# Optimization experiments

Hardware: AMD Instinct MI355X
Metric: run time of the kernel (lower is better)

The kernel has to match this reference:

```python
import jax, jax.numpy as jnp
import numpy as np

MUL = 128                      # shared multiplicity (MACE channels)
IN_DIMS = (1, 3, 5)            # 0e, 1o, 2e -> d_in_single = 9
OUT_DIMS = (1, 3)              # 0e, 1o -> d_out_single = 4
OUT_SLICES = ((0, 1), (1, 4))
ENTRIES = ((1, 0), (1, 1), (2, 0), (2, 1), (3, 0), (3, 1))  # (nu, out_idx)
N_BASIS = (1, 1, 2, 2, 3, 3)
N_NODES = 2048
N_ELEM = 10


def _to_per_mul(x):
    # (n, sum mul*dim) -> (n, mul, d_in_single)
    n = x.shape[0]
    pieces, off = [], 0
    for d in IN_DIMS:
        pieces.append(x[:, off:off + MUL * d].reshape(n, MUL, d))
        off += MUL * d
    return jnp.concatenate(pieces, axis=-1)


def _from_per_mul(x):
    # (n, mul, d_out_single) -> (n, sum mul*dim)
    n = x.shape[0]
    pieces = []
    for (lo, hi), d in zip(OUT_SLICES, OUT_DIMS):
        pieces.append(x[:, :, lo:hi].reshape(n, MUL * d))
    return jnp.concatenate(pieces, axis=-1)


def _symmetric_contraction(feats, species, bases, weights):
    n = feats.shape[0]
    out = jnp.zeros((n, MUL, sum(OUT_DIMS)), dtype=feats.dtype)
    for (nu, out_idx), basis, w in zip(ENTRIES, bases, weights):
        basis = jax.lax.stop_gradient(basis).astype(feats.dtype)
        # chain of nu symmetric contractions of basis against feats
        tmp = jnp.einsum('a...,ima->im...', basis, feats)  # (n, mul, 9^{nu-1}, nb, d)
        for _ in range(nu - 1):
            tmp = jnp.einsum('ima...,ima->im...', tmp, feats)
        w_per_node = w[species]                           # (n, nb, mul)
        contracted = jnp.einsum('nsm,nmsp->nmp', w_per_node, tmp)
        lo, hi = OUT_SLICES[out_idx]
        out = out.at[:, :, lo:hi].add(contracted)
    return out


def setup_inputs() -> dict:
    key = jax.random.key(0)
    ks = jax.random.split(key, 16)
    d_in = sum(IN_DIMS)
    inp = {
        'node_feats': jax.random.normal(ks[0], (N_NODES, MUL * d_in), jnp.float32),
        'species': jax.random.randint(ks[1], (N_NODES,), 0, N_ELEM),
    }
    names_b = ('b10', 'b11', 'b20', 'b21', 'b30', 'b31')
    names_w = ('w10', 'w11', 'w20', 'w21', 'w30', 'w31')
    for i, ((nu, oi), nb) in enumerate(zip(ENTRIES, N_BASIS)):
        bshape = (d_in,) * nu + (nb, OUT_DIMS[oi])
        inp[names_b[i]] = jax.random.normal(ks[2 + i], bshape, jnp.float32)
        scale = 1.0 / np.sqrt(nb)
        inp[names_w[i]] = jax.random.normal(ks[8 + i], (N_ELEM, nb, MUL), jnp.float32) * scale
    return inp


def reference(node_feats, species, b10, b11, b20, b21, b30, b31,
              w10, w11, w20, w21, w30, w31):
    feats = _to_per_mul(node_feats)
    out = _symmetric_contraction(
        feats, species,
        [b10, b11, b20, b21, b30, b31],
        [w10, w11, w20, w21, w30, w31])
    return _from_per_mul(out)
```

## Files before the change

### kernel.cpp

```cpp
#include <hip/hip_runtime.h>

#define NTH 256
#define N_NODES 2048

#define G3_OFF 0
#define G2_OFF 1980
#define G1_OFF 2340
#define TAB_FLOATS 2376

__global__ void mace_prep(
    const float* __restrict__ b10, const float* __restrict__ b11,
    const float* __restrict__ b20, const float* __restrict__ b21,
    const float* __restrict__ b30, const float* __restrict__ b31,
    float* __restrict__ tab)
{
    const int tid = threadIdx.x;
    if (tid < 165) {
        int i = 0, j = 0, k = 0;
        {
            int c = 0;
            for (int ii = 0; ii < 9; ii++)
                for (int jj = ii; jj < 9; jj++)
                    for (int kk = jj; kk < 9; kk++) {
                        if (c == tid) { i = ii; j = jj; k = kk; }
                        c++;
                    }
        }
        float s[12];
        #pragma unroll
        for (int q = 0; q < 12; q++) s[q] = 0.f;
        auto add3 = [&](int a, int b, int c2) {
            int o30 = ((a * 9 + b) * 9 + c2) * 3;
            int o31 = o30 * 3;
            #pragma unroll
            for (int q = 0; q < 3; q++) s[q] += b30[o30 + q];
            #pragma unroll
            for (int q = 0; q < 9; q++) s[3 + q] += b31[o31 + q];
        };
        if (i == j && j == k) { add3(i, j, k); }
        else if (i == j)      { add3(i, i, k); add3(i, k, i); add3(k, i, i); }
        else if (j == k)      { add3(i, j, j); add3(j, i, j); add3(j, j, i); }
        else { add3(i,j,k); add3(i,k,j); add3(j,i,k); add3(j,k,i); add3(k,i,j); add3(k,j,i); }
        #pragma unroll
        for (int q = 0; q < 12; q++) tab[G3_OFF + tid * 12 + q] = s[q];
    } else if (tid < 210) {
        int t = tid - 165;
        int i = 0, j = 0;
        {
            int c = 0;
            for (int ii = 0; ii < 9; ii++)
                for (int jj = ii; jj < 9; jj++) {
                    if (c == t) { i = ii; j = jj; }
                    c++;
                }
        }
        float s[8];
        #pragma unroll
        for (int q = 0; q < 8; q++) s[q] = 0.f;
        auto add2 = [&](int a, int b) {
            int o20 = (a * 9 + b) * 2;
            int o21 = o20 * 3;
            #pragma unroll
            for (int q = 0; q < 2; q++) s[q] += b20[o20 + q];
            #pragma unroll
            for (int q = 0; q < 6; q++) s[2 + q] += b21[o21 + q];
        };
        if (i == j) add2(i, i); else { add2(i, j); add2(j, i); }
        #pragma unroll
        for (int q = 0; q < 8; q++) tab[G2_OFF + t * 8 + q] = s[q];
    } else if (tid < 219) {
        int a = tid - 210;
        tab[G1_OFF + a * 4 + 0] = b10[a];
        #pragma unroll
        for (int p = 0; p < 3; p++) tab[G1_OFF + a * 4 + 1 + p] = b11[a * 3 + p];
    }
}

__global__ __launch_bounds__(NTH, 2) void mace_sc_kernel(
    const float* __restrict__ nf, const int* __restrict__ spec,
    const float* __restrict__ w10, const float* __restrict__ w11,
    const float* __restrict__ w20, const float* __restrict__ w21,
    const float* __restrict__ w30, const float* __restrict__ w31,
    const float* __restrict__ tab, float* __restrict__ out)
{
    const int g    = blockIdx.x * NTH + threadIdx.x;
    const int node = g >> 7;
    const int m    = g & 127;

    const float* nfp = nf + node * 1152;
    float f[9];
    f[0] = nfp[m];
    #pragma unroll
    for (int j = 0; j < 3; j++) f[1 + j] = nfp[128 + m * 3 + j];
    #pragma unroll
    for (int j = 0; j < 5; j++) f[4 + j] = nfp[512 + m * 5 + j];

    const int z = spec[node];

    float acc[4];
    #pragma unroll
    for (int p = 0; p < 4; p++) acc[p] = 0.f;

    {
        float t3[12];
        #pragma unroll
        for (int q = 0; q < 12; q++) t3[q] = 0.f;

        int t = 0;
        #pragma unroll
        for (int i = 0; i < 9; i++) {
            #pragma unroll
            for (int j = i; j < 9; j++) {
                const float fij = f[i] * f[j];
                #pragma unroll
                for (int k = j; k < 9; k++) {
                    const float* c = &tab[G3_OFF + t * 12];
                    const float m3 = fij * f[k];
                    #pragma unroll
                    for (int q = 0; q < 12; q++) t3[q] = fmaf(c[q], m3, t3[q]);
                    t++;
                }
            }
        }
        const float* w30z = w30 + z * 3 * 128;
        const float* w31z = w31 + z * 3 * 128;
        #pragma unroll
        for (int s = 0; s < 3; s++) {
            const float wv = w30z[s * 128 + m];
            acc[0] = fmaf(wv, t3[s], acc[0]);
            const float wu = w31z[s * 128 + m];
            acc[1] = fmaf(wu, t3[3 + s * 3 + 0], acc[1]);
            acc[2] = fmaf(wu, t3[3 + s * 3 + 1], acc[2]);
            acc[3] = fmaf(wu, t3[3 + s * 3 + 2], acc[3]);
        }
    }

    {
        float t2[8];
        #pragma unroll
        for (int q = 0; q < 8; q++) t2[q] = 0.f;

        int t = 0;
        #pragma unroll
        for (int i = 0; i < 9; i++) {
            #pragma unroll
            for (int j = i; j < 9; j++) {
                const float* c = &tab[G2_OFF + t * 8];
                const float m2 = f[i] * f[j];
                #pragma unroll
                for (int q = 0; q < 8; q++) t2[q] = fmaf(c[q], m2, t2[q]);
                t++;
            }
        }
        const float* w20z = w20 + z * 2 * 128;
        const float* w21z = w21 + z * 2 * 128;
        #pragma unroll
        for (int s = 0; s < 2; s++) {
            const float wv = w20z[s * 128 + m];
            acc[0] = fmaf(wv, t2[s], acc[0]);
            const float wu = w21z[s * 128 + m];
            acc[1] = fmaf(wu, t2[2 + s * 3 + 0], acc[1]);
            acc[2] = fmaf(wu, t2[2 + s * 3 + 1], acc[2]);
            acc[3] = fmaf(wu, t2[2 + s * 3 + 2], acc[3]);
        }
    }

    {
        float t1[4];
        #pragma unroll
        for (int q = 0; q < 4; q++) t1[q] = 0.f;

        #pragma unroll
        for (int a = 0; a < 9; a++) {
            const float* c = &tab[G1_OFF + a * 4];
            #pragma unroll
            for (int q = 0; q < 4; q++) t1[q] = fmaf(c[q], f[a], t1[q]);
        }
        const float wv = w10[z * 128 + m];
        acc[0] = fmaf(wv, t1[0], acc[0]);
        const float wu = w11[z * 128 + m];
        acc[1] = fmaf(wu, t1[1], acc[1]);
        acc[2] = fmaf(wu, t1[2], acc[2]);
        acc[3] = fmaf(wu, t1[3], acc[3]);
    }

    float* op = out + node * 512;
    op[m] = acc[0];
    #pragma unroll
    for (int p = 0; p < 3; p++) op[128 + m * 3 + p] = acc[1 + p];
}

extern "C" void kernel_launch(void* const* d_in, const int* in_sizes, int n_in,
                              void* d_out, int out_size, void* d_ws, size_t ws_size,
                              hipStream_t stream) {
    const float* nf  = (const float*)d_in[0];
    const int* spec  = (const int*)d_in[1];
    const float* b10 = (const float*)d_in[2];
    const float* w10 = (const float*)d_in[3];
    const float* b11 = (const float*)d_in[4];
    const float* w11 = (const float*)d_in[5];
    const float* b20 = (const float*)d_in[6];
    const float* w20 = (const float*)d_in[7];
    const float* b21 = (const float*)d_in[8];
    const float* w21 = (const float*)d_in[9];
    const float* b30 = (const float*)d_in[10];
    const float* w30 = (const float*)d_in[11];
    const float* b31 = (const float*)d_in[12];
    const float* w31 = (const float*)d_in[13];
    float* out = (float*)d_out;
    float* tab = (float*)d_ws;

    mace_prep<<<1, 256, 0, stream>>>(b10, b11, b20, b21, b30, b31, tab);

    const int n_threads = N_NODES * 128;
    const int grid = n_threads / NTH;
    mace_sc_kernel<<<grid, NTH, 0, stream>>>(
        nf, spec, w10, w11, w20, w21, w30, w31, tab, out);
}
```

Before: 116.7 us.

## Split output channels across two thread halves per node with shared-memory reduction

Each node now gets a 256-thread block, and two threads share each channel. Each thread computes half of the combined coefficient table columns (6 of 12 for nu=3, 4 of 8 for nu=2, 2 of 4 for nu=1), and the prep kernel writes the tables in split A/B halves to match. Partial accumulators from the second half are reduced through shared memory before the first half writes the output. This doubles the thread count, cuts per-thread FMA work and register pressure, and adds occupancy, at the cost of recomputing the monomials twice, loading the features twice, and one block barrier.

```diff
diff --git a/kernel.cpp b/kernel.cpp
--- a/kernel.cpp
+++ b/kernel.cpp
@@ -3,9 +3,12 @@
 #define NTH 256
 #define N_NODES 2048
 
-#define G3_OFF 0
-#define G2_OFF 1980
-#define G1_OFF 2340
+#define G3A_OFF 0
+#define G3B_OFF 990
+#define G2A_OFF 1980
+#define G2B_OFF 2160
+#define G1A_OFF 2340
+#define G1B_OFF 2358
 #define TAB_FLOATS 2376
 
 __global__ void mace_prep(
@@ -42,7 +45,10 @@
         else if (j == k)      { add3(i, j, j); add3(j, i, j); add3(j, j, i); }
         else { add3(i,j,k); add3(i,k,j); add3(j,i,k); add3(j,k,i); add3(k,i,j); add3(k,j,i); }
         #pragma unroll
-        for (int q = 0; q < 12; q++) tab[G3_OFF + tid * 12 + q] = s[q];
+        for (int q = 0; q < 6; q++) {
+            tab[G3A_OFF + tid * 6 + q] = s[q];
+            tab[G3B_OFF + tid * 6 + q] = s[6 + q];
+        }
     } else if (tid < 210) {
         int t = tid - 165;
         int i = 0, j = 0;
@@ -67,12 +73,16 @@
         };
         if (i == j) add2(i, i); else { add2(i, j); add2(j, i); }
         #pragma unroll
-        for (int q = 0; q < 8; q++) tab[G2_OFF + t * 8 + q] = s[q];
+        for (int q = 0; q < 4; q++) {
+            tab[G2A_OFF + t * 4 + q] = s[q];
+            tab[G2B_OFF + t * 4 + q] = s[4 + q];
+        }
     } else if (tid < 219) {
         int a = tid - 210;
-        tab[G1_OFF + a * 4 + 0] = b10[a];
-        #pragma unroll
-        for (int p = 0; p < 3; p++) tab[G1_OFF + a * 4 + 1 + p] = b11[a * 3 + p];
+        tab[G1A_OFF + a * 2 + 0] = b10[a];
+        tab[G1A_OFF + a * 2 + 1] = b11[a * 3 + 0];
+        tab[G1B_OFF + a * 2 + 0] = b11[a * 3 + 1];
+        tab[G1B_OFF + a * 2 + 1] = b11[a * 3 + 2];
     }
 }
 
@@ -83,9 +93,13 @@
     const float* __restrict__ w30, const float* __restrict__ w31,
     const float* __restrict__ tab, float* __restrict__ out)
 {
-    const int g    = blockIdx.x * NTH + threadIdx.x;
-    const int node = g >> 7;
-    const int m    = g & 127;
+    __shared__ float part[4][128];
+
+    const int node = blockIdx.x;
+    const int tid  = threadIdx.x;
+    const int w    = tid >> 6;
+    const int h    = w >> 1;
+    const int m    = ((w & 1) << 6) | (tid & 63);
 
     const float* nfp = nf + node * 1152;
     float f[9];
@@ -102,9 +116,10 @@
     for (int p = 0; p < 4; p++) acc[p] = 0.f;
 
     {
-        float t3[12];
-        #pragma unroll
-        for (int q = 0; q < 12; q++) t3[q] = 0.f;
+        const float* g3 = tab + (h ? G3B_OFF : G3A_OFF);
+        float t3[6];
+        #pragma unroll
+        for (int q = 0; q < 6; q++) t3[q] = 0.f;
 
         int t = 0;
         #pragma unroll
@@ -114,80 +129,107 @@
                 const float fij = f[i] * f[j];
                 #pragma unroll
                 for (int k = j; k < 9; k++) {
-                    const float* c = &tab[G3_OFF + t * 12];
+                    const float* c = &g3[t * 6];
                     const float m3 = fij * f[k];
                     #pragma unroll
-                    for (int q = 0; q < 12; q++) t3[q] = fmaf(c[q], m3, t3[q]);
+                    for (int q = 0; q < 6; q++) t3[q] = fmaf(c[q], m3, t3[q]);
                     t++;
                 }
             }
         }
-        const float* w30z = w30 + z * 3 * 128;
-        const float* w31z = w31 + z * 3 * 128;
-        #pragma unroll
-        for (int s = 0; s < 3; s++) {
-            const float wv = w30z[s * 128 + m];
-            acc[0] = fmaf(wv, t3[s], acc[0]);
-            const float wu = w31z[s * 128 + m];
-            acc[1] = fmaf(wu, t3[3 + s * 3 + 0], acc[1]);
-            acc[2] = fmaf(wu, t3[3 + s * 3 + 1], acc[2]);
-            acc[3] = fmaf(wu, t3[3 + s * 3 + 2], acc[3]);
+        if (h == 0) {
+            const float* w30z = w30 + z * 384;
+            const float* w31z = w31 + z * 384;
+            #pragma unroll
+            for (int s = 0; s < 3; s++)
+                acc[0] = fmaf(w30z[s * 128 + m], t3[s], acc[0]);
+            const float wu = w31z[m];
+            acc[1] = fmaf(wu, t3[3], acc[1]);
+            acc[2] = fmaf(wu, t3[4], acc[2]);
+            acc[3] = fmaf(wu, t3[5], acc[3]);
+        } else {
+            const float* w31z = w31 + z * 384;
+            const float wu1 = w31z[128 + m];
+            const float wu2 = w31z[256 + m];
+            acc[1] = fmaf(wu1, t3[0], acc[1]);
+            acc[2] = fmaf(wu1, t3[1], acc[2]);
+            acc[3] = fmaf(wu1, t3[2], acc[3]);
+            acc[1] = fmaf(wu2, t3[3], acc[1]);
+            acc[2] = fmaf(wu2, t3[4], acc[2]);
+            acc[3] = fmaf(wu2, t3[5], acc[3]);
         }
     }
 
     {
-        float t2[8];
-        #pragma unroll
-        for (int q = 0; q < 8; q++) t2[q] = 0.f;
+        const float* g2 = tab + (h ? G2B_OFF : G2A_OFF);
+        float t2[4];
+        #pragma unroll
+        for (int q = 0; q < 4; q++) t2[q] = 0.f;
 
         int t = 0;
         #pragma unroll
         for (int i = 0; i < 9; i++) {
             #pragma unroll
             for (int j = i; j < 9; j++) {
-                const float* c = &tab[G2_OFF + t * 8];
+                const float* c = &g2[t * 4];
                 const float m2 = f[i] * f[j];
                 #pragma unroll
-                for (int q = 0; q < 8; q++) t2[q] = fmaf(c[q], m2, t2[q]);
+                for (int q = 0; q < 4; q++) t2[q] = fmaf(c[q], m2, t2[q]);
                 t++;
             }
         }
-        const float* w20z = w20 + z * 2 * 128;
-        const float* w21z = w21 + z * 2 * 128;
-        #pragma unroll
-        for (int s = 0; s < 2; s++) {
-            const float wv = w20z[s * 128 + m];
-            acc[0] = fmaf(wv, t2[s], acc[0]);
-            const float wu = w21z[s * 128 + m];
-            acc[1] = fmaf(wu, t2[2 + s * 3 + 0], acc[1]);
-            acc[2] = fmaf(wu, t2[2 + s * 3 + 1], acc[2]);
-            acc[3] = fmaf(wu, t2[2 + s * 3 + 2], acc[3]);
+        if (h == 0) {
+            const float* w20z = w20 + z * 256;
+            const float* w21z = w21 + z * 256;
+            acc[0] = fmaf(w20z[m],       t2[0], acc[0]);
+            acc[0] = fmaf(w20z[128 + m], t2[1], acc[0]);
+            const float wu = w21z[m];
+            acc[1] = fmaf(wu, t2[2], acc[1]);
+            acc[2] = fmaf(wu, t2[3], acc[2]);
+        } else {
+            const float* w21z = w21 + z * 256;
+            const float wu0 = w21z[m];
+            acc[3] = fmaf(wu0, t2[0], acc[3]);
+            const float wu1 = w21z[128 + m];
+            acc[1] = fmaf(wu1, t2[1], acc[1]);
+            acc[2] = fmaf(wu1, t2[2], acc[2]);
+            acc[3] = fmaf(wu1, t2[3], acc[3]);
         }
     }
 
     {
-        float t1[4];
-        #pragma unroll
-        for (int q = 0; q < 4; q++) t1[q] = 0.f;
-
+        const float* g1 = tab + (h ? G1B_OFF : G1A_OFF);
+        float t1[2];
+        t1[0] = 0.f; t1[1] = 0.f;
         #pragma unroll
         for (int a = 0; a < 9; a++) {
-            const float* c = &tab[G1_OFF + a * 4];
-            #pragma unroll
-            for (int q = 0; q < 4; q++) t1[q] = fmaf(c[q], f[a], t1[q]);
-        }
-        const float wv = w10[z * 128 + m];
-        acc[0] = fmaf(wv, t1[0], acc[0]);
-        const float wu = w11[z * 128 + m];
-        acc[1] = fmaf(wu, t1[1], acc[1]);
-        acc[2] = fmaf(wu, t1[2], acc[2]);
-        acc[3] = fmaf(wu, t1[3], acc[3]);
-    }
-
-    float* op = out + node * 512;
-    op[m] = acc[0];
-    #pragma unroll
-    for (int p = 0; p < 3; p++) op[128 + m * 3 + p] = acc[1 + p];
+            const float* c = &g1[a * 2];
+            t1[0] = fmaf(c[0], f[a], t1[0]);
+            t1[1] = fmaf(c[1], f[a], t1[1]);
+        }
+        if (h == 0) {
+            acc[0] = fmaf(w10[z * 128 + m], t1[0], acc[0]);
+            acc[1] = fmaf(w11[z * 128 + m], t1[1], acc[1]);
+        } else {
+            const float wu = w11[z * 128 + m];
+            acc[2] = fmaf(wu, t1[0], acc[2]);
+            acc[3] = fmaf(wu, t1[1], acc[3]);
+        }
+    }
+
+    if (h == 1) {
+        #pragma unroll
+        for (int p = 0; p < 4; p++) part[p][m] = acc[p];
+    }
+    __syncthreads();
+    if (h == 0) {
+        #pragma unroll
+        for (int p = 0; p < 4; p++) acc[p] += part[p][m];
+        float* op = out + node * 512;
+        op[m] = acc[0];
+        #pragma unroll
+        for (int p = 0; p < 3; p++) op[128 + m * 3 + p] = acc[1 + p];
+    }
 }
 
 extern "C" void kernel_launch(void* const* d_in, const int* in_sizes, int n_in,
@@ -212,8 +254,6 @@
 
     mace_prep<<<1, 256, 0, stream>>>(b10, b11, b20, b21, b30, b31, tab);
 
-    const int n_threads = N_NODES * 128;
-    const int grid = n_threads / NTH;
-    mace_sc_kernel<<<grid, NTH, 0, stream>>>(
+    mace_sc_kernel<<<N_NODES, NTH, 0, stream>>>(
         nf, spec, w10, w11, w20, w21, w30, w31, tab, out);
 }
```

New measurement: 160.1 us. 1.37x slower.
